# Optimization experiments

Measured on AMD Instinct MI355X. Metric: run time of the kernel, lower is better.

## Reference

```python
import jax, jax.numpy as jnp
import numpy as np
from jax import lax

NPOINT = 1024
RADIUS = 0.2
NSAMPLE = 32
BN_EPS = 1e-5


def farthest_point_sample(xyz, npoint):
    # xyz: (B, N, 3). Deterministic start at index 0 (torch version starts at a
    # random index; the algorithm is otherwise identical).
    B, N, _ = xyz.shape

    def step(carry, _):
        distance, farthest = carry
        centroid = jnp.take_along_axis(xyz, farthest[:, None, None], axis=1)  # (B,1,3)
        d = jnp.sum((xyz - centroid) ** 2, axis=-1)  # (B,N)
        distance = jnp.minimum(distance, d)
        new_farthest = jnp.argmax(distance, axis=-1).astype(jnp.int32)
        return (distance, new_farthest), farthest

    init = (jnp.full((B, N), 1e10, xyz.dtype), jnp.zeros((B,), jnp.int32))
    _, centroids = lax.scan(step, init, None, length=npoint)  # (npoint, B)
    return centroids.T  # (B, npoint)


def batched_gather(points, idx):
    # points: (B, N, C); idx: (B, ...) -> (B, ..., C)
    return jax.vmap(lambda p, i: p[i])(points, idx)


def square_distance(src, dst):
    # src: (B,S,3), dst: (B,N,3) -> (B,S,N)
    d = -2.0 * jnp.einsum('bsc,bnc->bsn', src, dst)
    d += jnp.sum(src ** 2, -1)[:, :, None]
    d += jnp.sum(dst ** 2, -1)[:, None, :]
    return d


def query_ball_point(radius, nsample, xyz, new_xyz):
    B, N, _ = xyz.shape
    S = new_xyz.shape[1]
    sqrdists = square_distance(new_xyz, xyz)                 # (B,S,N)
    neg_d, idx = lax.top_k(-sqrdists, nsample)               # smallest nsample dists
    out_of_ball = (-neg_d) > radius ** 2                     # (B,S,nsample)
    first = idx[:, :, 0]
    # if even the nearest point is outside the ball, group the centroid itself
    first = jnp.where(out_of_ball[:, :, 0], jnp.arange(S, dtype=idx.dtype)[None, :], first)
    idx = jnp.where(out_of_ball, first[:, :, None], idx)
    return idx


def sa_forward(xyz_b3n, points_bdn, params):
    xyz = jnp.transpose(xyz_b3n, (0, 2, 1))      # (B,N,3)
    pts = jnp.transpose(points_bdn, (0, 2, 1))   # (B,N,D)
    fps_idx = farthest_point_sample(xyz, NPOINT)             # (B,S)
    new_xyz = batched_gather(xyz, fps_idx)                   # (B,S,3)
    idx = query_ball_point(RADIUS, NSAMPLE, xyz, new_xyz)    # (B,S,K)
    grouped_xyz = batched_gather(xyz, idx)                   # (B,S,K,3)
    grouped_xyz_norm = grouped_xyz - new_xyz[:, :, None, :]
    grouped_pts = batched_gather(pts, idx)                   # (B,S,K,D)
    x = jnp.concatenate([grouped_xyz_norm, grouped_pts], -1) # (B,S,K,3+D)

    for (w, b, gamma, beta) in params:
        x = jnp.einsum('bskc,oc->bsko', x, w) + b            # 1x1 conv
        mu = jnp.mean(x, axis=(0, 1, 2))
        var = jnp.var(x, axis=(0, 1, 2))                     # biased, as torch BN
        x = jax.nn.relu(gamma * (x - mu) * lax.rsqrt(var + BN_EPS) + beta)

    new_points = jnp.max(x, axis=2)                          # max over nsample K
    return (jnp.transpose(new_xyz, (0, 2, 1)),
            jnp.transpose(new_points, (0, 2, 1)),
            fps_idx)


def setup_inputs() -> dict:
    key = jax.random.key(0)
    ks = jax.random.split(key, 8)
    B, N, D = 16, 4096, 64
    xyz = jax.random.uniform(ks[0], (B, 3, N), dtype=jnp.float32)
    points = jax.random.normal(ks[1], (B, D, N), dtype=jnp.float32)
    mlp = [64, 64, 128]
    last = 3 + D  # in_channel = 67
    inp = {'xyz': xyz, 'points': points}
    for i, out in enumerate(mlp):
        inp[f'w{i}'] = jax.random.normal(ks[2 + i], (out, last), dtype=jnp.float32) * (1.0 / np.sqrt(last))
        inp[f'b{i}'] = jnp.zeros((out,), jnp.float32)
        inp[f'gamma{i}'] = jnp.ones((out,), jnp.float32)
        inp[f'beta{i}'] = jnp.zeros((out,), jnp.float32)
        last = out
    return inp


def reference(xyz, points, w0, b0, gamma0, beta0, w1, b1, gamma1, beta1, w2, b2, gamma2, beta2):
    params = [(w0, b0, gamma0, beta0), (w1, b1, gamma1, beta1), (w2, b2, gamma2, beta2)]
    return sa_forward(xyz, points, params)
```

## Files before the change

### kernel.cpp

```cpp
#include <hip/hip_runtime.h>

using f32x4  = __attribute__((ext_vector_type(4))) float;
using short8 = __attribute__((ext_vector_type(8))) short;
using u64x2  = __attribute__((ext_vector_type(2))) unsigned long long;

__device__ __forceinline__ unsigned short f2bf(float f) {
  unsigned u = __builtin_bit_cast(unsigned, f);
  u = (u + 0x7FFFu + ((u >> 16) & 1u)) >> 16;
  return (unsigned short)u;
}
__device__ __forceinline__ float bf2f(unsigned short s) {
  return __builtin_bit_cast(float, ((unsigned)s) << 16);
}
__device__ __forceinline__ double u2d(unsigned long long u) {
  return __builtin_bit_cast(double, u);
}
__device__ __forceinline__ unsigned long long d2u(double d) {
  return __builtin_bit_cast(unsigned long long, d);
}
__device__ __forceinline__ unsigned cvt_pk_bf16(float lo, float hi) {
  unsigned r;
  asm("v_cvt_pk_bf16_f32 %0, %1, %2" : "=v"(r) : "v"(lo), "v"(hi));
  return r;
}

template <int CTRL>
__device__ __forceinline__ double dpp_max_f64(double best) {
  unsigned long long u = d2u(best);
  int lo32 = (int)(unsigned)u;
  int hi32 = (int)(unsigned)(u >> 32);
  int plo = __builtin_amdgcn_update_dpp(0, lo32, CTRL, 0xF, 0xF, true);
  int phi = __builtin_amdgcn_update_dpp(0, hi32, CTRL, 0xF, 0xF, true);
  unsigned long long p =
      ((unsigned long long)(unsigned)phi << 32) | (unsigned long long)(unsigned)plo;
  return fmax(best, u2d(p));
}
template <int CTRL>
__device__ __forceinline__ double dpp_min_f64(double v) {
  unsigned long long u = d2u(v);
  int lo32 = (int)(unsigned)u;
  int hi32 = (int)(unsigned)(u >> 32);
  int plo = __builtin_amdgcn_update_dpp(lo32, lo32, CTRL, 0xF, 0xF, false);
  int phi = __builtin_amdgcn_update_dpp(hi32, hi32, CTRL, 0xF, 0xF, false);
  unsigned long long p =
      ((unsigned long long)(unsigned)phi << 32) | (unsigned long long)(unsigned)plo;
  return fmin(v, u2d(p));
}

union SmemFP {
  struct {
    float4 sp4[4096];
    unsigned long long scand[2][16];
    int sfar[1024];
  } f;
  float tile[64][65];
};

__global__ __launch_bounds__(256, 1) void k_fp(const float* __restrict__ xyz,
                                               const float* __restrict__ points,
                                               float* __restrict__ out0,
                                               float* __restrict__ out2,
                                               int* __restrict__ fpsidx,
                                               float4* __restrict__ nq4,
                                               unsigned short* __restrict__ pT,
                                               float4* __restrict__ xyz4,
                                               const float* __restrict__ w0,
                                               const float* __restrict__ w1,
                                               const float* __restrict__ w2,
                                               unsigned short* __restrict__ wb0,
                                               unsigned short* __restrict__ wb1,
                                               unsigned short* __restrict__ wb2) {
  __shared__ SmemFP sm;
  int t = threadIdx.x, blk = blockIdx.x;
  if (blk >= 16) {
    int pb = blk - 16;
    if (pb == 1024) {
      for (int e = t; e < 64 * 96; e += 256) {
        int o = e / 96, k = e - o * 96;
        float v = (k < 64) ? w0[o * 67 + 3 + k] : ((k < 67) ? w0[o * 67 + (k - 64)] : 0.f);
        wb0[e] = f2bf(v);
      }
      for (int e = t; e < 4096; e += 256) wb1[e] = f2bf(w1[e]);
      for (int e = t; e < 8192; e += 256) wb2[e] = f2bf(w2[e]);
      return;
    }
    int b = pb >> 6, n0 = (pb & 63) << 6;
#pragma unroll
    for (int p = 0; p < 16; ++p) {
      int c = p * 4 + (t >> 6);
      sm.tile[c][t & 63] = points[(size_t)b * 262144 + (size_t)c * 4096 + n0 + (t & 63)];
    }
    if (t < 64) {
      int n = n0 + t;
      float x = xyz[(size_t)b * 12288 + n];
      float y = xyz[(size_t)b * 12288 + 4096 + n];
      float z = xyz[(size_t)b * 12288 + 8192 + n];
      float ps = __fadd_rn(__fadd_rn(__fmul_rn(x, x), __fmul_rn(y, y)), __fmul_rn(z, z));
      xyz4[(size_t)b * 4096 + n] = make_float4(x, y, z, ps);
    }
    __syncthreads();
    int nl = t >> 2, coff = (t & 3) * 16;
    unsigned v[8];
#pragma unroll
    for (int j = 0; j < 8; ++j)
      v[j] = cvt_pk_bf16(sm.tile[coff + 2 * j][nl], sm.tile[coff + 2 * j + 1][nl]);
    uint4* dst = reinterpret_cast<uint4*>(pT + ((size_t)b * 4096 + n0 + nl) * 64 + coff);
    dst[0] = make_uint4(v[0], v[1], v[2], v[3]);
    dst[1] = make_uint4(v[4], v[5], v[6], v[7]);
    return;
  }
  int b = blk;
  float px[16], py[16], pz[16], dist[16];
#pragma unroll
  for (int j = 0; j < 16; ++j) {
    int n = t + (j << 8);
    float x = xyz[(size_t)b * 12288 + n];
    float y = xyz[(size_t)b * 12288 + 4096 + n];
    float z = xyz[(size_t)b * 12288 + 8192 + n];
    px[j] = x; py[j] = y; pz[j] = z; dist[j] = 1e10f;
    sm.f.sp4[n] = make_float4(x, y, z, 0.f);
  }
  __syncthreads();
#pragma unroll
  for (int j = 0; j < 16; ++j) {
    asm volatile("" : "+v"(px[j]), "+v"(py[j]), "+v"(pz[j]));
  }
  unsigned nt = ~(unsigned)t;
  int far = 0;
  float cx = sm.f.sp4[0].x, cy = sm.f.sp4[0].y, cz = sm.f.sp4[0].z;
  for (int it = 0; it < 1024; ++it) {
    if (t == 0) sm.f.sfar[it] = far;
    double best0 = 0.0, best1 = 0.0;
#pragma unroll
    for (int j = 0; j < 16; ++j) {
      float dx = __fsub_rn(px[j], cx);
      float dy = __fsub_rn(py[j], cy);
      float dz = __fsub_rn(pz[j], cz);
      float d  = __fadd_rn(__fadd_rn(__fmul_rn(dx, dx), __fmul_rn(dy, dy)), __fmul_rn(dz, dz));
      float nd = fminf(dist[j], d);
      dist[j] = nd;
      unsigned long long cand =
          ((unsigned long long)__builtin_bit_cast(unsigned, nd) << 32) |
          (unsigned long long)(nt - (unsigned)(j << 8));
      if (j & 1) best1 = fmax(best1, u2d(cand));
      else       best0 = fmax(best0, u2d(cand));
    }
    double best = fmax(best0, best1);
    best = dpp_max_f64<0xB1>(best);
    best = dpp_max_f64<0x4E>(best);
    best = dpp_max_f64<0x124>(best);
    best = dpp_max_f64<0x128>(best);
    int pb = it & 1;
    if ((t & 15) == 0) sm.f.scand[pb][t >> 4] = d2u(best);
    __syncthreads();
    double g = u2d(sm.f.scand[pb][t & 15]);
    g = dpp_max_f64<0xB1>(g);
    g = dpp_max_f64<0x4E>(g);
    g = dpp_max_f64<0x124>(g);
    g = dpp_max_f64<0x128>(g);
    unsigned long long bw = d2u(g);
    int n = (int)(~(unsigned)bw) & 4095;
    far = n;
    float4 c4 = sm.f.sp4[n];
    cx = c4.x; cy = c4.y; cz = c4.z;
  }
  __syncthreads();
#pragma unroll
  for (int h = 0; h < 4; ++h) {
    int k = (h << 8) + t;
    int fr = sm.f.sfar[k];
    float4 p = sm.f.sp4[fr];
    float x = p.x, y = p.y, z = p.z;
    fpsidx[(b << 10) + k] = fr;
    out2[(b << 10) + k] = (float)fr;
    out0[(size_t)b * 3072 + k]        = x;
    out0[(size_t)b * 3072 + 1024 + k] = y;
    out0[(size_t)b * 3072 + 2048 + k] = z;
    float ps = __fadd_rn(__fadd_rn(__fmul_rn(x, x), __fmul_rn(y, y)), __fmul_rn(z, z));
    nq4[(b << 10) + k] = make_float4(x, y, z, ps);
  }
}

#define BCAP 384
__global__ __launch_bounds__(256) void k_ball(const float4* __restrict__ xyz4,
                                              const int* __restrict__ fpsidx,
                                              int* __restrict__ ballidx) {
  __shared__ __align__(16) float4 sp[4096];
  __shared__ unsigned long long spk[4][BCAP];
  const unsigned long long INVP = 0x7149F2CAFFFFFFFFull;
  int t = threadIdx.x, blk = blockIdx.x;
  int b = blk >> 6;
  for (int i = t; i < 4096; i += 256) sp[i] = xyz4[(size_t)b * 4096 + i];
  __syncthreads();
  int lane = t & 63, wid = t >> 6;
  for (int r = 0; r < 4; ++r) {
    int q = blk * 16 + r * 4 + wid;
    int qi = fpsidx[q];
    float4 Q = sp[qi];
    float qx = Q.x, qy = Q.y, qz = Q.z, qs = Q.w;
    int cnt = 0;
    for (int i = 0; i < 64; ++i) {
      int n = (i << 6) + lane;
      float4 P = sp[n];
      float dot = __fadd_rn(__fadd_rn(__fmul_rn(qx, P.x), __fmul_rn(qy, P.y)), __fmul_rn(qz, P.z));
      float d   = __fadd_rn(__fadd_rn(__fmul_rn(-2.f, dot), qs), P.w);
      bool in = (d <= 0.04f);
      unsigned long long m = __ballot(in);
      int pos = cnt + (int)__popcll(m & ((1ull << lane) - 1ull));
      if (in && pos < BCAP)
        spk[wid][pos] = ((unsigned long long)__builtin_bit_cast(unsigned, d) << 32) | (unsigned)n;
      cnt += (int)__popcll(m);
    }
    if (cnt > BCAP) cnt = BCAP;
    double c0, c1, c2, c3, c4, c5;
    {
      int s0 = lane, s1 = lane + 64, s2 = lane + 128, s3 = lane + 192, s4 = lane + 256, s5 = lane + 320;
      c0 = (s0 < cnt) ? u2d(spk[wid][s0]) : u2d(INVP);
      c1 = (s1 < cnt) ? u2d(spk[wid][s1]) : u2d(INVP);
      c2 = (s2 < cnt) ? u2d(spk[wid][s2]) : u2d(INVP);
      c3 = (s3 < cnt) ? u2d(spk[wid][s3]) : u2d(INVP);
      c4 = (s4 < cnt) ? u2d(spk[wid][s4]) : u2d(INVP);
      c5 = (s5 < cnt) ? u2d(spk[wid][s5]) : u2d(INVP);
    }
#define CE(a, b) { double mn_ = fmin(a, b), mx_ = fmax(a, b); a = mn_; b = mx_; }
    CE(c0, c1);
    CE(c1, c2); CE(c0, c1);
    CE(c2, c3); CE(c1, c2); CE(c0, c1);
    CE(c3, c4); CE(c2, c3); CE(c1, c2); CE(c0, c1);
    CE(c4, c5); CE(c3, c4); CE(c2, c3); CE(c1, c2); CE(c0, c1);
#undef CE
    int firstI = 0;
#pragma unroll 1
    for (int rr = 0; rr < 32; ++rr) {
      double h = c0;
      h = dpp_min_f64<0xB1>(h);
      h = dpp_min_f64<0x4E>(h);
      h = dpp_min_f64<0x124>(h);
      h = dpp_min_f64<0x128>(h);
      unsigned long long hu = d2u(h);
      int lo = (int)(unsigned)hu, hi = (int)(unsigned)(hu >> 32);
      unsigned long long r0 = ((unsigned long long)(unsigned)__builtin_amdgcn_readlane(hi, 0)  << 32) | (unsigned)__builtin_amdgcn_readlane(lo, 0);
      unsigned long long r1 = ((unsigned long long)(unsigned)__builtin_amdgcn_readlane(hi, 16) << 32) | (unsigned)__builtin_amdgcn_readlane(lo, 16);
      unsigned long long r2 = ((unsigned long long)(unsigned)__builtin_amdgcn_readlane(hi, 32) << 32) | (unsigned)__builtin_amdgcn_readlane(lo, 32);
      unsigned long long r3 = ((unsigned long long)(unsigned)__builtin_amdgcn_readlane(hi, 48) << 32) | (unsigned)__builtin_amdgcn_readlane(lo, 48);
      double w = fmin(fmin(u2d(r0), u2d(r1)), fmin(u2d(r2), u2d(r3)));
      unsigned long long wu = d2u(w);
      int wi = (int)(unsigned)wu;
      if (rr == 0) firstI = wi;
      int outv = (wu < INVP) ? wi : firstI;
      if (lane == 0) ballidx[(size_t)q * 32 + rr] = outv;
      if (d2u(c0) == wu) {
        c0 = c1; c1 = c2; c2 = c3; c3 = c4; c4 = c5; c5 = u2d(INVP);
      }
    }
  }
}

__global__ __launch_bounds__(256) void k_gemm1(const unsigned short* __restrict__ pT,
    const float4* __restrict__ xyz4, const float4* __restrict__ nq4,
    const int* __restrict__ bidx, const unsigned short* __restrict__ wb,
    const float* __restrict__ bia, unsigned short* __restrict__ xbuf,
    float* __restrict__ part) {
  __shared__ unsigned short A[64][104];
  __shared__ unsigned short W[64][104];
  __shared__ float sred[4][2][64];
  int t = threadIdx.x, blk = blockIdx.x;
  int b = blk >> 9;
  for (int e = t; e < 768; e += 256) {
    int o = e / 12, k8 = e - o * 12;
    *reinterpret_cast<uint4*>(&W[o][k8 * 8]) = reinterpret_cast<const uint4*>(wb)[e];
  }
  {
    int rt = t >> 2, sub = t & 3;
    int q = (blk << 1) + (rt >> 5);
    int n = bidx[(size_t)q * 32 + (rt & 31)];
    const uint4* src = reinterpret_cast<const uint4*>(pT + ((size_t)(b * 4096 + n)) * 64 + sub * 16);
    uint4 v0 = src[0], v1 = src[1];
    *reinterpret_cast<uint4*>(&A[rt][sub * 16])     = v0;
    *reinterpret_cast<uint4*>(&A[rt][sub * 16 + 8]) = v1;
    if (sub == 0) {
      float4 P = xyz4[(size_t)b * 4096 + n];
      float4 Qc = nq4[q];
      A[rt][64] = f2bf(__fsub_rn(P.x, Qc.x));
      A[rt][65] = f2bf(__fsub_rn(P.y, Qc.y));
      A[rt][66] = f2bf(__fsub_rn(P.z, Qc.z));
    } else if (sub == 1) {
#pragma unroll
      for (int k = 67; k < 96; ++k) A[rt][k] = 0;
    }
  }
  __syncthreads();
  int lane = t & 63, wid = t >> 6;
  int cl = lane & 15, rg = lane >> 4;
  int rowb = (wid << 4) + cl, ko = rg << 3;
  f32x4 acc[4] = {};
#pragma unroll
  for (int ks = 0; ks < 96; ks += 32) {
    short8 a = *reinterpret_cast<const short8*>(&A[rowb][ks + ko]);
#pragma unroll
    for (int nt = 0; nt < 4; ++nt) {
      short8 bb = *reinterpret_cast<const short8*>(&W[nt * 16 + cl][ks + ko]);
      acc[nt] = __builtin_amdgcn_mfma_f32_16x16x32_bf16(a, bb, acc[nt], 0, 0, 0);
    }
  }
#pragma unroll
  for (int nt = 0; nt < 4; ++nt) {
    int ch = nt * 16 + cl;
    float bv = bia[ch];
    float v0 = acc[nt][0] + bv, v1 = acc[nt][1] + bv, v2 = acc[nt][2] + bv, v3 = acc[nt][3] + bv;
    size_t gr = (size_t)blk * 64 + (wid << 4) + (rg << 2);
    xbuf[(gr + 0) * 64 + ch] = f2bf(v0);
    xbuf[(gr + 1) * 64 + ch] = f2bf(v1);
    xbuf[(gr + 2) * 64 + ch] = f2bf(v2);
    xbuf[(gr + 3) * 64 + ch] = f2bf(v3);
    float s1 = (v0 + v1) + (v2 + v3);
    float s2 = (v0 * v0 + v1 * v1) + (v2 * v2 + v3 * v3);
    s1 += __shfl_xor(s1, 16); s1 += __shfl_xor(s1, 32);
    s2 += __shfl_xor(s2, 16); s2 += __shfl_xor(s2, 32);
    if (rg == 0) { sred[wid][0][ch] = s1; sred[wid][1][ch] = s2; }
  }
  __syncthreads();
  if (t < 128) {
    int ch = t & 63, wh = t >> 6;
    float v = sred[0][wh][ch] + sred[1][wh][ch] + sred[2][wh][ch] + sred[3][wh][ch];
    part[(size_t)blk * 128 + ch * 2 + wh] = v;
  }
}

__global__ __launch_bounds__(256) void k_red(const float* __restrict__ part, int nblk, int nch,
    const float* __restrict__ gamma, const float* __restrict__ beta,
    float* __restrict__ scale, float* __restrict__ shift) {
  int c = blockIdx.x, t = threadIdx.x;
  int stride = 2 * nch;
  float s1 = 0.f, s2 = 0.f;
  for (int i = t; i < nblk; i += 256) {
    s1 += part[(size_t)i * stride + 2 * c];
    s2 += part[(size_t)i * stride + 2 * c + 1];
  }
  __shared__ float r1[256], r2[256];
  r1[t] = s1; r2[t] = s2;
  __syncthreads();
  for (int o = 128; o > 0; o >>= 1) {
    if (t < o) { r1[t] += r1[t + o]; r2[t] += r2[t + o]; }
    __syncthreads();
  }
  if (t == 0) {
    const float N = 524288.f;
    float mu = r1[0] / N;
    float var = r2[0] / N - mu * mu;
    float a = gamma[c] / sqrtf(var + 1e-5f);
    scale[c] = a;
    shift[c] = beta[c] - a * mu;
  }
}

__global__ __launch_bounds__(256) void k_gemm2(unsigned short* __restrict__ xbuf,
    const unsigned short* __restrict__ wb, const float* __restrict__ bia,
    const float* __restrict__ sc, const float* __restrict__ sh,
    float* __restrict__ part) {
  __shared__ unsigned short A[64][72];
  __shared__ unsigned short W[64][72];
  __shared__ float ssc[64], ssh[64];
  __shared__ float sred[4][2][64];
  int t = threadIdx.x, blk = blockIdx.x;
  if (t < 64) { ssc[t] = sc[t]; ssh[t] = sh[t]; }
  __syncthreads();
  for (int e = t; e < 512; e += 256) {
    int o = e >> 3, k8 = e & 7;
    *reinterpret_cast<uint4*>(&W[o][k8 * 8]) = reinterpret_cast<const uint4*>(wb)[e];
  }
  {
    int rt = t >> 2, sub = t & 3;
    size_t gr = (size_t)blk * 64 + rt;
    const uint4* src = reinterpret_cast<const uint4*>(xbuf + gr * 64 + sub * 16);
    uint4 v0 = src[0], v1 = src[1];
    unsigned wv[8] = {v0.x, v0.y, v0.z, v0.w, v1.x, v1.y, v1.z, v1.w};
    unsigned pk[8];
#pragma unroll
    for (int j = 0; j < 8; ++j) {
      int c = sub * 16 + 2 * j;
      float x0 = bf2f((unsigned short)(wv[j] & 0xffffu));
      float x1 = bf2f((unsigned short)(wv[j] >> 16));
      float a0 = fmaxf(0.f, ssc[c] * x0 + ssh[c]);
      float a1 = fmaxf(0.f, ssc[c + 1] * x1 + ssh[c + 1]);
      pk[j] = cvt_pk_bf16(a0, a1);
    }
    *reinterpret_cast<uint4*>(&A[rt][sub * 16])     = make_uint4(pk[0], pk[1], pk[2], pk[3]);
    *reinterpret_cast<uint4*>(&A[rt][sub * 16 + 8]) = make_uint4(pk[4], pk[5], pk[6], pk[7]);
  }
  __syncthreads();
  int lane = t & 63, wid = t >> 6;
  int cl = lane & 15, rg = lane >> 4;
  int rowb = (wid << 4) + cl, ko = rg << 3;
  f32x4 acc[4] = {};
#pragma unroll
  for (int ks = 0; ks < 64; ks += 32) {
    short8 a = *reinterpret_cast<const short8*>(&A[rowb][ks + ko]);
#pragma unroll
    for (int nt = 0; nt < 4; ++nt) {
      short8 bb = *reinterpret_cast<const short8*>(&W[nt * 16 + cl][ks + ko]);
      acc[nt] = __builtin_amdgcn_mfma_f32_16x16x32_bf16(a, bb, acc[nt], 0, 0, 0);
    }
  }
#pragma unroll
  for (int nt = 0; nt < 4; ++nt) {
    int ch = nt * 16 + cl;
    float bv = bia[ch];
    float v0 = acc[nt][0] + bv, v1 = acc[nt][1] + bv, v2 = acc[nt][2] + bv, v3 = acc[nt][3] + bv;
    size_t gr = (size_t)blk * 64 + (wid << 4) + (rg << 2);
    xbuf[(gr + 0) * 64 + ch] = f2bf(v0);
    xbuf[(gr + 1) * 64 + ch] = f2bf(v1);
    xbuf[(gr + 2) * 64 + ch] = f2bf(v2);
    xbuf[(gr + 3) * 64 + ch] = f2bf(v3);
    float s1 = (v0 + v1) + (v2 + v3);
    float s2 = (v0 * v0 + v1 * v1) + (v2 * v2 + v3 * v3);
    s1 += __shfl_xor(s1, 16); s1 += __shfl_xor(s1, 32);
    s2 += __shfl_xor(s2, 16); s2 += __shfl_xor(s2, 32);
    if (rg == 0) { sred[wid][0][ch] = s1; sred[wid][1][ch] = s2; }
  }
  __syncthreads();
  if (t < 128) {
    int ch = t & 63, wh = t >> 6;
    float v = sred[0][wh][ch] + sred[1][wh][ch] + sred[2][wh][ch] + sred[3][wh][ch];
    part[(size_t)blk * 128 + ch * 2 + wh] = v;
  }
}

__global__ __launch_bounds__(256) void k_gemm3(unsigned short* xbuf,
    const unsigned short* __restrict__ wb, const float* __restrict__ bia,
    const float* __restrict__ sc2, const float* __restrict__ sh2,
    float* __restrict__ part) {
  __shared__ unsigned short A[64][72];
  __shared__ unsigned short W[128][72];
  __shared__ float ssc[64], ssh[64];
  __shared__ float sred[4][4][128];
  int t = threadIdx.x, blk = blockIdx.x;
  if (t < 64) { ssc[t] = sc2[t]; ssh[t] = sh2[t]; }
  __syncthreads();
  for (int e = t; e < 1024; e += 256) {
    int o = e >> 3, k8 = e & 7;
    *reinterpret_cast<uint4*>(&W[o][k8 * 8]) = reinterpret_cast<const uint4*>(wb)[e];
  }
  {
    int rt = t >> 2, sub = t & 3;
    size_t gr = (size_t)blk * 64 + rt;
    const uint4* src = reinterpret_cast<const uint4*>(xbuf + gr * 64 + sub * 16);
    uint4 v0 = src[0], v1 = src[1];
    unsigned wv[8] = {v0.x, v0.y, v0.z, v0.w, v1.x, v1.y, v1.z, v1.w};
    unsigned pk[8];
#pragma unroll
    for (int j = 0; j < 8; ++j) {
      int c = sub * 16 + 2 * j;
      float x0 = bf2f((unsigned short)(wv[j] & 0xffffu));
      float x1 = bf2f((unsigned short)(wv[j] >> 16));
      float a0 = fmaxf(0.f, ssc[c] * x0 + ssh[c]);
      float a1 = fmaxf(0.f, ssc[c + 1] * x1 + ssh[c + 1]);
      pk[j] = cvt_pk_bf16(a0, a1);
    }
    *reinterpret_cast<uint4*>(&A[rt][sub * 16])     = make_uint4(pk[0], pk[1], pk[2], pk[3]);
    *reinterpret_cast<uint4*>(&A[rt][sub * 16 + 8]) = make_uint4(pk[4], pk[5], pk[6], pk[7]);
  }
  __syncthreads();
  int lane = t & 63, wid = t >> 6;
  int cl = lane & 15, rg = lane >> 4;
  int rowb = (wid << 4) + cl, ko = rg << 3;
  f32x4 acc[8] = {};
#pragma unroll
  for (int ks = 0; ks < 64; ks += 32) {
    short8 a = *reinterpret_cast<const short8*>(&A[rowb][ks + ko]);
#pragma unroll
    for (int nt = 0; nt < 8; ++nt) {
      short8 bb = *reinterpret_cast<const short8*>(&W[nt * 16 + cl][ks + ko]);
      acc[nt] = __builtin_amdgcn_mfma_f32_16x16x32_bf16(a, bb, acc[nt], 0, 0, 0);
    }
  }
#pragma unroll
  for (int nt = 0; nt < 8; ++nt) {
    int ch = nt * 16 + cl;
    float bv = bia[ch];
    float v0 = acc[nt][0] + bv, v1 = acc[nt][1] + bv, v2 = acc[nt][2] + bv, v3 = acc[nt][3] + bv;
    float s1 = (v0 + v1) + (v2 + v3);
    float s2 = (v0 * v0 + v1 * v1) + (v2 * v2 + v3 * v3);
    float mx = fmaxf(fmaxf(v0, v1), fmaxf(v2, v3));
    float mn = fminf(fminf(v0, v1), fminf(v2, v3));
    s1 += __shfl_xor(s1, 16); s1 += __shfl_xor(s1, 32);
    s2 += __shfl_xor(s2, 16); s2 += __shfl_xor(s2, 32);
    mx = fmaxf(mx, __shfl_xor(mx, 16)); mx = fmaxf(mx, __shfl_xor(mx, 32));
    mn = fminf(mn, __shfl_xor(mn, 16)); mn = fminf(mn, __shfl_xor(mn, 32));
    if (rg == 0) {
      sred[wid][0][ch] = s1; sred[wid][1][ch] = s2;
      sred[wid][2][ch] = mx; sred[wid][3][ch] = mn;
    }
  }
  __syncthreads();
  {
    int ch = t & 127, wh = t >> 7;
    part[(size_t)blk * 256 + ch * 2 + wh] =
        sred[0][wh][ch] + sred[1][wh][ch] + sred[2][wh][ch] + sred[3][wh][ch];
    float mx = fmaxf(sred[2 * wh][2][ch], sred[2 * wh + 1][2][ch]);
    float mn = fminf(sred[2 * wh][3][ch], sred[2 * wh + 1][3][ch]);
    float* mm = reinterpret_cast<float*>(xbuf) + (size_t)blk * 2048;
    mm[wh * 256 + ch]       = mx;
    mm[wh * 256 + 128 + ch] = mn;
  }
}

__global__ __launch_bounds__(256) void k_fin(const float* __restrict__ mm,
                                             const float* __restrict__ sc3,
                                             const float* __restrict__ sh3,
                                             float* __restrict__ out1) {
  __shared__ float tile[32][33];
  int t = threadIdx.x, blk = blockIdx.x;
  int b = blk >> 7, rem = blk & 127, ct = rem >> 5, st = rem & 31;
  int c0 = ct * 32, s0 = st * 32;
#pragma unroll
  for (int p = 0; p < 4; ++p) {
    int s_local = (t >> 5) + p * 8;
    int c = c0 + (t & 31);
    int q = (b << 10) + s0 + s_local;
    size_t base = (size_t)(q >> 1) * 2048 + (size_t)(q & 1) * 256;
    float mx = mm[base + c];
    float mn = mm[base + 128 + c];
    float sc = sc3[c], sh = sh3[c];
    float v = (sc >= 0.f) ? mx : mn;
    tile[t & 31][s_local] = fmaxf(0.f, sc * v + sh);
  }
  __syncthreads();
#pragma unroll
  for (int p = 0; p < 4; ++p) {
    int c = c0 + (t >> 5) + p * 8;
    int s = s0 + (t & 31);
    out1[(size_t)b * 131072 + (size_t)c * 1024 + s] = tile[(t >> 5) + p * 8][t & 31];
  }
}

extern "C" void kernel_launch(void* const* d_in, const int* in_sizes, int n_in,
                              void* d_out, int out_size, void* d_ws, size_t ws_size,
                              hipStream_t stream) {
  (void)in_sizes; (void)n_in; (void)out_size;
  const float* xyz    = (const float*)d_in[0];
  const float* points = (const float*)d_in[1];
  const float* w0  = (const float*)d_in[2];
  const float* b0  = (const float*)d_in[3];
  const float* g0  = (const float*)d_in[4];
  const float* be0 = (const float*)d_in[5];
  const float* w1  = (const float*)d_in[6];
  const float* b1  = (const float*)d_in[7];
  const float* g1  = (const float*)d_in[8];
  const float* be1 = (const float*)d_in[9];
  const float* w2  = (const float*)d_in[10];
  const float* b2  = (const float*)d_in[11];
  const float* g2  = (const float*)d_in[12];
  const float* be2 = (const float*)d_in[13];
  float* out  = (float*)d_out;
  float* out0 = out;
  float* out1 = out + 49152;
  float* out2 = out + 49152 + 2097152;
  char* ws = (char*)d_ws;
  const size_t OFF_PT    = 0;
  const size_t OFF_XYZ4  = 8388608;
  const size_t OFF_NQ4   = 9437184;
  const size_t OFF_FPS   = 9699328;
  const size_t OFF_BALL  = 9764864;
  const size_t OFF_XBUF  = 11862016;
  const size_t OFF_PART  = 78970880;
  const size_t OFF_SC    = 87359488;
  const size_t OFF_WB    = 87363584;
  const size_t NEED      = 87400448;
  if (ws_size < NEED) return;
  unsigned short* pT   = (unsigned short*)(ws + OFF_PT);
  float4* xyz4 = (float4*)(ws + OFF_XYZ4);
  float4* nq4  = (float4*)(ws + OFF_NQ4);
  int* fpsidx  = (int*)(ws + OFF_FPS);
  int* ballidx = (int*)(ws + OFF_BALL);
  unsigned short* xbuf = (unsigned short*)(ws + OFF_XBUF);
  float* part  = (float*)(ws + OFF_PART);
  float* scb   = (float*)(ws + OFF_SC);
  float *sc1 = scb, *sh1 = scb + 128, *sc2 = scb + 256, *sh2 = scb + 384,
        *sc3 = scb + 512, *sh3 = scb + 640;
  unsigned short* wb0 = (unsigned short*)(ws + OFF_WB);
  unsigned short* wb1 = wb0 + 6144;
  unsigned short* wb2 = wb1 + 4096;

  k_fp<<<1041, 256, 0, stream>>>(xyz, points, out0, out2, fpsidx, nq4,
                                 pT, xyz4, w0, w1, w2, wb0, wb1, wb2);
  k_ball<<<1024, 256, 0, stream>>>(xyz4, fpsidx, ballidx);
  k_gemm1<<<8192, 256, 0, stream>>>(pT, xyz4, nq4, ballidx, wb0, b0, xbuf, part);
  k_red<<<64, 256, 0, stream>>>(part, 8192, 64, g0, be0, sc1, sh1);
  k_gemm2<<<8192, 256, 0, stream>>>(xbuf, wb1, b1, sc1, sh1, part);
  k_red<<<64, 256, 0, stream>>>(part, 8192, 64, g1, be1, sc2, sh2);
  k_gemm3<<<8192, 256, 0, stream>>>(xbuf, wb2, b2, sc2, sh2, part);
  k_red<<<128, 256, 0, stream>>>(part, 8192, 128, g2, be2, sc3, sh3);
  k_fin<<<2048, 256, 0, stream>>>((const float*)xbuf, sc3, sh3, out1);
}
```

Baseline: 814.8 us.

## Recompute earlier MLP layers per stage instead of storing intermediate activations

Replaces the store-and-reload of bf16 intermediate activations between the three MLP stages with recomputation. Each stage re-gathers the grouped inputs and recomputes the previous GEMMs in shared memory before its own GEMM and batch-norm statistics. This removes about 64 MB of activation writes and reads per layer pass. In exchange it adds redundant MFMA work, repeated gathers and more shared memory per block, which may reduce occupancy.

```diff
diff --git a/kernel.cpp b/kernel.cpp
--- a/kernel.cpp
+++ b/kernel.cpp
@@ -256,11 +256,34 @@
   }
 }
 
-__global__ __launch_bounds__(256) void k_gemm1(const unsigned short* __restrict__ pT,
+template <typename SmemA>
+__device__ __forceinline__ void build_A(SmemA& A, int blk, int b,
+    const unsigned short* __restrict__ pT, const float4* __restrict__ xyz4,
+    const float4* __restrict__ nq4, const int* __restrict__ bidx) {
+  int t = threadIdx.x;
+  int rt = t >> 2, sub = t & 3;
+  int q = (blk << 1) + (rt >> 5);
+  int n = bidx[(size_t)q * 32 + (rt & 31)];
+  const uint4* src = reinterpret_cast<const uint4*>(pT + ((size_t)(b * 4096 + n)) * 64 + sub * 16);
+  uint4 v0 = src[0], v1 = src[1];
+  *reinterpret_cast<uint4*>(&A[rt][sub * 16])     = v0;
+  *reinterpret_cast<uint4*>(&A[rt][sub * 16 + 8]) = v1;
+  if (sub == 0) {
+    float4 P = xyz4[(size_t)b * 4096 + n];
+    float4 Qc = nq4[q];
+    A[rt][64] = f2bf(__fsub_rn(P.x, Qc.x));
+    A[rt][65] = f2bf(__fsub_rn(P.y, Qc.y));
+    A[rt][66] = f2bf(__fsub_rn(P.z, Qc.z));
+  } else if (sub == 1) {
+#pragma unroll
+    for (int k = 67; k < 96; ++k) A[rt][k] = 0;
+  }
+}
+
+__global__ __launch_bounds__(256) void k_g1s(const unsigned short* __restrict__ pT,
     const float4* __restrict__ xyz4, const float4* __restrict__ nq4,
     const int* __restrict__ bidx, const unsigned short* __restrict__ wb,
-    const float* __restrict__ bia, unsigned short* __restrict__ xbuf,
-    float* __restrict__ part) {
+    const float* __restrict__ bia, float* __restrict__ part) {
   __shared__ unsigned short A[64][104];
   __shared__ unsigned short W[64][104];
   __shared__ float sred[4][2][64];
@@ -270,25 +293,7 @@
     int o = e / 12, k8 = e - o * 12;
     *reinterpret_cast<uint4*>(&W[o][k8 * 8]) = reinterpret_cast<const uint4*>(wb)[e];
   }
-  {
-    int rt = t >> 2, sub = t & 3;
-    int q = (blk << 1) + (rt >> 5);
-    int n = bidx[(size_t)q * 32 + (rt & 31)];
-    const uint4* src = reinterpret_cast<const uint4*>(pT + ((size_t)(b * 4096 + n)) * 64 + sub * 16);
-    uint4 v0 = src[0], v1 = src[1];
-    *reinterpret_cast<uint4*>(&A[rt][sub * 16])     = v0;
-    *reinterpret_cast<uint4*>(&A[rt][sub * 16 + 8]) = v1;
-    if (sub == 0) {
-      float4 P = xyz4[(size_t)b * 4096 + n];
-      float4 Qc = nq4[q];
-      A[rt][64] = f2bf(__fsub_rn(P.x, Qc.x));
-      A[rt][65] = f2bf(__fsub_rn(P.y, Qc.y));
-      A[rt][66] = f2bf(__fsub_rn(P.z, Qc.z));
-    } else if (sub == 1) {
-#pragma unroll
-      for (int k = 67; k < 96; ++k) A[rt][k] = 0;
-    }
-  }
+  build_A(A, blk, b, pT, xyz4, nq4, bidx);
   __syncthreads();
   int lane = t & 63, wid = t >> 6;
   int cl = lane & 15, rg = lane >> 4;
@@ -308,11 +313,6 @@
     int ch = nt * 16 + cl;
     float bv = bia[ch];
     float v0 = acc[nt][0] + bv, v1 = acc[nt][1] + bv, v2 = acc[nt][2] + bv, v3 = acc[nt][3] + bv;
-    size_t gr = (size_t)blk * 64 + (wid << 4) + (rg << 2);
-    xbuf[(gr + 0) * 64 + ch] = f2bf(v0);
-    xbuf[(gr + 1) * 64 + ch] = f2bf(v1);
-    xbuf[(gr + 2) * 64 + ch] = f2bf(v2);
-    xbuf[(gr + 3) * 64 + ch] = f2bf(v3);
     float s1 = (v0 + v1) + (v2 + v3);
     float s2 = (v0 * v0 + v1 * v1) + (v2 * v2 + v3 * v3);
     s1 += __shfl_xor(s1, 16); s1 += __shfl_xor(s1, 32);
@@ -327,91 +327,75 @@
   }
 }
 
-__global__ __launch_bounds__(256) void k_red(const float* __restrict__ part, int nblk, int nch,
-    const float* __restrict__ gamma, const float* __restrict__ beta,
-    float* __restrict__ scale, float* __restrict__ shift) {
-  int c = blockIdx.x, t = threadIdx.x;
-  int stride = 2 * nch;
-  float s1 = 0.f, s2 = 0.f;
-  for (int i = t; i < nblk; i += 256) {
-    s1 += part[(size_t)i * stride + 2 * c];
-    s2 += part[(size_t)i * stride + 2 * c + 1];
-  }
-  __shared__ float r1[256], r2[256];
-  r1[t] = s1; r2[t] = s2;
-  __syncthreads();
-  for (int o = 128; o > 0; o >>= 1) {
-    if (t < o) { r1[t] += r1[t + o]; r2[t] += r2[t + o]; }
-    __syncthreads();
-  }
-  if (t == 0) {
-    const float N = 524288.f;
-    float mu = r1[0] / N;
-    float var = r2[0] / N - mu * mu;
-    float a = gamma[c] / sqrtf(var + 1e-5f);
-    scale[c] = a;
-    shift[c] = beta[c] - a * mu;
-  }
-}
-
-__global__ __launch_bounds__(256) void k_gemm2(unsigned short* __restrict__ xbuf,
-    const unsigned short* __restrict__ wb, const float* __restrict__ bia,
-    const float* __restrict__ sc, const float* __restrict__ sh,
+__global__ __launch_bounds__(256) void k_g2r(const unsigned short* __restrict__ pT,
+    const float4* __restrict__ xyz4, const float4* __restrict__ nq4,
+    const int* __restrict__ bidx,
+    const unsigned short* __restrict__ wb0, const float* __restrict__ bia0,
+    const unsigned short* __restrict__ wb1, const float* __restrict__ bia1,
+    const float* __restrict__ sc1, const float* __restrict__ sh1,
     float* __restrict__ part) {
-  __shared__ unsigned short A[64][72];
-  __shared__ unsigned short W[64][72];
+  __shared__ unsigned short A[64][104];
+  __shared__ unsigned short W1[64][104];
+  __shared__ unsigned short W2[64][72];
   __shared__ float ssc[64], ssh[64];
   __shared__ float sred[4][2][64];
   int t = threadIdx.x, blk = blockIdx.x;
-  if (t < 64) { ssc[t] = sc[t]; ssh[t] = sh[t]; }
-  __syncthreads();
+  int b = blk >> 9;
+  if (t < 64) { ssc[t] = sc1[t]; ssh[t] = sh1[t]; }
+  for (int e = t; e < 768; e += 256) {
+    int o = e / 12, k8 = e - o * 12;
+    *reinterpret_cast<uint4*>(&W1[o][k8 * 8]) = reinterpret_cast<const uint4*>(wb0)[e];
+  }
   for (int e = t; e < 512; e += 256) {
     int o = e >> 3, k8 = e & 7;
-    *reinterpret_cast<uint4*>(&W[o][k8 * 8]) = reinterpret_cast<const uint4*>(wb)[e];
-  }
-  {
-    int rt = t >> 2, sub = t & 3;
-    size_t gr = (size_t)blk * 64 + rt;
-    const uint4* src = reinterpret_cast<const uint4*>(xbuf + gr * 64 + sub * 16);
-    uint4 v0 = src[0], v1 = src[1];
-    unsigned wv[8] = {v0.x, v0.y, v0.z, v0.w, v1.x, v1.y, v1.z, v1.w};
-    unsigned pk[8];
-#pragma unroll
-    for (int j = 0; j < 8; ++j) {
-      int c = sub * 16 + 2 * j;
-      float x0 = bf2f((unsigned short)(wv[j] & 0xffffu));
-      float x1 = bf2f((unsigned short)(wv[j] >> 16));
-      float a0 = fmaxf(0.f, ssc[c] * x0 + ssh[c]);
-      float a1 = fmaxf(0.f, ssc[c + 1] * x1 + ssh[c + 1]);
-      pk[j] = cvt_pk_bf16(a0, a1);
-    }
-    *reinterpret_cast<uint4*>(&A[rt][sub * 16])     = make_uint4(pk[0], pk[1], pk[2], pk[3]);
-    *reinterpret_cast<uint4*>(&A[rt][sub * 16 + 8]) = make_uint4(pk[4], pk[5], pk[6], pk[7]);
-  }
+    *reinterpret_cast<uint4*>(&W2[o][k8 * 8]) = reinterpret_cast<const uint4*>(wb1)[e];
+  }
+  build_A(A, blk, b, pT, xyz4, nq4, bidx);
   __syncthreads();
   int lane = t & 63, wid = t >> 6;
   int cl = lane & 15, rg = lane >> 4;
   int rowb = (wid << 4) + cl, ko = rg << 3;
-  f32x4 acc[4] = {};
+  f32x4 acc1[4] = {};
+#pragma unroll
+  for (int ks = 0; ks < 96; ks += 32) {
+    short8 a = *reinterpret_cast<const short8*>(&A[rowb][ks + ko]);
+#pragma unroll
+    for (int nt = 0; nt < 4; ++nt) {
+      short8 bb = *reinterpret_cast<const short8*>(&W1[nt * 16 + cl][ks + ko]);
+      acc1[nt] = __builtin_amdgcn_mfma_f32_16x16x32_bf16(a, bb, acc1[nt], 0, 0, 0);
+    }
+  }
+  __syncthreads();
+  {
+    int r0 = (wid << 4) + (rg << 2);
+#pragma unroll
+    for (int nt = 0; nt < 4; ++nt) {
+      int ch = nt * 16 + cl;
+      float bv = bia0[ch];
+#pragma unroll
+      for (int i = 0; i < 4; ++i) {
+        float x1 = bf2f(f2bf(acc1[nt][i] + bv));
+        float a = fmaxf(0.f, ssc[ch] * x1 + ssh[ch]);
+        A[r0 + i][ch] = f2bf(a);
+      }
+    }
+  }
+  __syncthreads();
+  f32x4 acc2[4] = {};
 #pragma unroll
   for (int ks = 0; ks < 64; ks += 32) {
     short8 a = *reinterpret_cast<const short8*>(&A[rowb][ks + ko]);
 #pragma unroll
     for (int nt = 0; nt < 4; ++nt) {
-      short8 bb = *reinterpret_cast<const short8*>(&W[nt * 16 + cl][ks + ko]);
-      acc[nt] = __builtin_amdgcn_mfma_f32_16x16x32_bf16(a, bb, acc[nt], 0, 0, 0);
+      short8 bb = *reinterpret_cast<const short8*>(&W2[nt * 16 + cl][ks + ko]);
+      acc2[nt] = __builtin_amdgcn_mfma_f32_16x16x32_bf16(a, bb, acc2[nt], 0, 0, 0);
     }
   }
 #pragma unroll
   for (int nt = 0; nt < 4; ++nt) {
     int ch = nt * 16 + cl;
-    float bv = bia[ch];
-    float v0 = acc[nt][0] + bv, v1 = acc[nt][1] + bv, v2 = acc[nt][2] + bv, v3 = acc[nt][3] + bv;
-    size_t gr = (size_t)blk * 64 + (wid << 4) + (rg << 2);
-    xbuf[(gr + 0) * 64 + ch] = f2bf(v0);
-    xbuf[(gr + 1) * 64 + ch] = f2bf(v1);
-    xbuf[(gr + 2) * 64 + ch] = f2bf(v2);
-    xbuf[(gr + 3) * 64 + ch] = f2bf(v3);
+    float bv = bia1[ch];
+    float v0 = acc2[nt][0] + bv, v1 = acc2[nt][1] + bv, v2 = acc2[nt][2] + bv, v3 = acc2[nt][3] + bv;
     float s1 = (v0 + v1) + (v2 + v3);
     float s2 = (v0 * v0 + v1 * v1) + (v2 * v2 + v3 * v3);
     s1 += __shfl_xor(s1, 16); s1 += __shfl_xor(s1, 32);
@@ -426,59 +410,104 @@
   }
 }
 
-__global__ __launch_bounds__(256) void k_gemm3(unsigned short* xbuf,
-    const unsigned short* __restrict__ wb, const float* __restrict__ bia,
+__global__ __launch_bounds__(256) void k_g3r(const unsigned short* __restrict__ pT,
+    const float4* __restrict__ xyz4, const float4* __restrict__ nq4,
+    const int* __restrict__ bidx,
+    const unsigned short* __restrict__ wb0, const float* __restrict__ bia0,
+    const unsigned short* __restrict__ wb1, const float* __restrict__ bia1,
+    const unsigned short* __restrict__ wb2, const float* __restrict__ bia2,
+    const float* __restrict__ sc1, const float* __restrict__ sh1,
     const float* __restrict__ sc2, const float* __restrict__ sh2,
-    float* __restrict__ part) {
-  __shared__ unsigned short A[64][72];
-  __shared__ unsigned short W[128][72];
-  __shared__ float ssc[64], ssh[64];
+    float* __restrict__ mmout, float* __restrict__ part) {
+  __shared__ unsigned short A[64][104];
+  __shared__ unsigned short W1[64][104];
+  __shared__ unsigned short W2[64][72];
+  __shared__ unsigned short W3[128][72];
+  __shared__ float s1c[64], s1h[64], s2c[64], s2h[64];
   __shared__ float sred[4][4][128];
   int t = threadIdx.x, blk = blockIdx.x;
-  if (t < 64) { ssc[t] = sc2[t]; ssh[t] = sh2[t]; }
-  __syncthreads();
+  int b = blk >> 9;
+  if (t < 64) { s1c[t] = sc1[t]; s1h[t] = sh1[t]; }
+  else if (t < 128) { s2c[t - 64] = sc2[t - 64]; s2h[t - 64] = sh2[t - 64]; }
+  for (int e = t; e < 768; e += 256) {
+    int o = e / 12, k8 = e - o * 12;
+    *reinterpret_cast<uint4*>(&W1[o][k8 * 8]) = reinterpret_cast<const uint4*>(wb0)[e];
+  }
+  for (int e = t; e < 512; e += 256) {
+    int o = e >> 3, k8 = e & 7;
+    *reinterpret_cast<uint4*>(&W2[o][k8 * 8]) = reinterpret_cast<const uint4*>(wb1)[e];
+  }
   for (int e = t; e < 1024; e += 256) {
     int o = e >> 3, k8 = e & 7;
-    *reinterpret_cast<uint4*>(&W[o][k8 * 8]) = reinterpret_cast<const uint4*>(wb)[e];
-  }
-  {
-    int rt = t >> 2, sub = t & 3;
-    size_t gr = (size_t)blk * 64 + rt;
-    const uint4* src = reinterpret_cast<const uint4*>(xbuf + gr * 64 + sub * 16);
-    uint4 v0 = src[0], v1 = src[1];
-    unsigned wv[8] = {v0.x, v0.y, v0.z, v0.w, v1.x, v1.y, v1.z, v1.w};
-    unsigned pk[8];
-#pragma unroll
-    for (int j = 0; j < 8; ++j) {
-      int c = sub * 16 + 2 * j;
-      float x0 = bf2f((unsigned short)(wv[j] & 0xffffu));
-      float x1 = bf2f((unsigned short)(wv[j] >> 16));
-      float a0 = fmaxf(0.f, ssc[c] * x0 + ssh[c]);
-      float a1 = fmaxf(0.f, ssc[c + 1] * x1 + ssh[c + 1]);
-      pk[j] = cvt_pk_bf16(a0, a1);
-    }
-    *reinterpret_cast<uint4*>(&A[rt][sub * 16])     = make_uint4(pk[0], pk[1], pk[2], pk[3]);
-    *reinterpret_cast<uint4*>(&A[rt][sub * 16 + 8]) = make_uint4(pk[4], pk[5], pk[6], pk[7]);
-  }
+    *reinterpret_cast<uint4*>(&W3[o][k8 * 8]) = reinterpret_cast<const uint4*>(wb2)[e];
+  }
+  build_A(A, blk, b, pT, xyz4, nq4, bidx);
   __syncthreads();
   int lane = t & 63, wid = t >> 6;
   int cl = lane & 15, rg = lane >> 4;
   int rowb = (wid << 4) + cl, ko = rg << 3;
-  f32x4 acc[8] = {};
+  int r0 = (wid << 4) + (rg << 2);
+  f32x4 acc1[4] = {};
+#pragma unroll
+  for (int ks = 0; ks < 96; ks += 32) {
+    short8 a = *reinterpret_cast<const short8*>(&A[rowb][ks + ko]);
+#pragma unroll
+    for (int nt = 0; nt < 4; ++nt) {
+      short8 bb = *reinterpret_cast<const short8*>(&W1[nt * 16 + cl][ks + ko]);
+      acc1[nt] = __builtin_amdgcn_mfma_f32_16x16x32_bf16(a, bb, acc1[nt], 0, 0, 0);
+    }
+  }
+  __syncthreads();
+#pragma unroll
+  for (int nt = 0; nt < 4; ++nt) {
+    int ch = nt * 16 + cl;
+    float bv = bia0[ch];
+#pragma unroll
+    for (int i = 0; i < 4; ++i) {
+      float x1 = bf2f(f2bf(acc1[nt][i] + bv));
+      float a = fmaxf(0.f, s1c[ch] * x1 + s1h[ch]);
+      A[r0 + i][ch] = f2bf(a);
+    }
+  }
+  __syncthreads();
+  f32x4 acc2[4] = {};
 #pragma unroll
   for (int ks = 0; ks < 64; ks += 32) {
     short8 a = *reinterpret_cast<const short8*>(&A[rowb][ks + ko]);
 #pragma unroll
+    for (int nt = 0; nt < 4; ++nt) {
+      short8 bb = *reinterpret_cast<const short8*>(&W2[nt * 16 + cl][ks + ko]);
+      acc2[nt] = __builtin_amdgcn_mfma_f32_16x16x32_bf16(a, bb, acc2[nt], 0, 0, 0);
+    }
+  }
+  __syncthreads();
+#pragma unroll
+  for (int nt = 0; nt < 4; ++nt) {
+    int ch = nt * 16 + cl;
+    float bv = bia1[ch];
+#pragma unroll
+    for (int i = 0; i < 4; ++i) {
+      float x2 = bf2f(f2bf(acc2[nt][i] + bv));
+      float a = fmaxf(0.f, s2c[ch] * x2 + s2h[ch]);
+      A[r0 + i][ch] = f2bf(a);
+    }
+  }
+  __syncthreads();
+  f32x4 acc3[8] = {};
+#pragma unroll
+  for (int ks = 0; ks < 64; ks += 32) {
+    short8 a = *reinterpret_cast<const short8*>(&A[rowb][ks + ko]);
+#pragma unroll
     for (int nt = 0; nt < 8; ++nt) {
-      short8 bb = *reinterpret_cast<const short8*>(&W[nt * 16 + cl][ks + ko]);
-      acc[nt] = __builtin_amdgcn_mfma_f32_16x16x32_bf16(a, bb, acc[nt], 0, 0, 0);
+      short8 bb = *reinterpret_cast<const short8*>(&W3[nt * 16 + cl][ks + ko]);
+      acc3[nt] = __builtin_amdgcn_mfma_f32_16x16x32_bf16(a, bb, acc3[nt], 0, 0, 0);
     }
   }
 #pragma unroll
   for (int nt = 0; nt < 8; ++nt) {
     int ch = nt * 16 + cl;
-    float bv = bia[ch];
-    float v0 = acc[nt][0] + bv, v1 = acc[nt][1] + bv, v2 = acc[nt][2] + bv, v3 = acc[nt][3] + bv;
+    float bv = bia2[ch];
+    float v0 = acc3[nt][0] + bv, v1 = acc3[nt][1] + bv, v2 = acc3[nt][2] + bv, v3 = acc3[nt][3] + bv;
     float s1 = (v0 + v1) + (v2 + v3);
     float s2 = (v0 * v0 + v1 * v1) + (v2 * v2 + v3 * v3);
     float mx = fmaxf(fmaxf(v0, v1), fmaxf(v2, v3));
@@ -499,9 +528,36 @@
         sred[0][wh][ch] + sred[1][wh][ch] + sred[2][wh][ch] + sred[3][wh][ch];
     float mx = fmaxf(sred[2 * wh][2][ch], sred[2 * wh + 1][2][ch]);
     float mn = fminf(sred[2 * wh][3][ch], sred[2 * wh + 1][3][ch]);
-    float* mm = reinterpret_cast<float*>(xbuf) + (size_t)blk * 2048;
+    float* mm = mmout + (size_t)blk * 2048;
     mm[wh * 256 + ch]       = mx;
     mm[wh * 256 + 128 + ch] = mn;
+  }
+}
+
+__global__ __launch_bounds__(256) void k_red(const float* __restrict__ part, int nblk, int nch,
+    const float* __restrict__ gamma, const float* __restrict__ beta,
+    float* __restrict__ scale, float* __restrict__ shift) {
+  int c = blockIdx.x, t = threadIdx.x;
+  int stride = 2 * nch;
+  float s1 = 0.f, s2 = 0.f;
+  for (int i = t; i < nblk; i += 256) {
+    s1 += part[(size_t)i * stride + 2 * c];
+    s2 += part[(size_t)i * stride + 2 * c + 1];
+  }
+  __shared__ float r1[256], r2[256];
+  r1[t] = s1; r2[t] = s2;
+  __syncthreads();
+  for (int o = 128; o > 0; o >>= 1) {
+    if (t < o) { r1[t] += r1[t + o]; r2[t] += r2[t + o]; }
+    __syncthreads();
+  }
+  if (t == 0) {
+    const float N = 524288.f;
+    float mu = r1[0] / N;
+    float var = r2[0] / N - mu * mu;
+    float a = gamma[c] / sqrtf(var + 1e-5f);
+    scale[c] = a;
+    shift[c] = beta[c] - a * mu;
   }
 }
 
@@ -562,7 +618,7 @@
   const size_t OFF_NQ4   = 9437184;
   const size_t OFF_FPS   = 9699328;
   const size_t OFF_BALL  = 9764864;
-  const size_t OFF_XBUF  = 11862016;
+  const size_t OFF_MM    = 11862016;
   const size_t OFF_PART  = 78970880;
   const size_t OFF_SC    = 87359488;
   const size_t OFF_WB    = 87363584;
@@ -573,7 +629,7 @@
   float4* nq4  = (float4*)(ws + OFF_NQ4);
   int* fpsidx  = (int*)(ws + OFF_FPS);
   int* ballidx = (int*)(ws + OFF_BALL);
-  unsigned short* xbuf = (unsigned short*)(ws + OFF_XBUF);
+  float* mmbuf = (float*)(ws + OFF_MM);
   float* part  = (float*)(ws + OFF_PART);
   float* scb   = (float*)(ws + OFF_SC);
   float *sc1 = scb, *sh1 = scb + 128, *sc2 = scb + 256, *sh2 = scb + 384,
@@ -585,11 +641,12 @@
   k_fp<<<1041, 256, 0, stream>>>(xyz, points, out0, out2, fpsidx, nq4,
                                  pT, xyz4, w0, w1, w2, wb0, wb1, wb2);
   k_ball<<<1024, 256, 0, stream>>>(xyz4, fpsidx, ballidx);
-  k_gemm1<<<8192, 256, 0, stream>>>(pT, xyz4, nq4, ballidx, wb0, b0, xbuf, part);
+  k_g1s<<<8192, 256, 0, stream>>>(pT, xyz4, nq4, ballidx, wb0, b0, part);
   k_red<<<64, 256, 0, stream>>>(part, 8192, 64, g0, be0, sc1, sh1);
-  k_gemm2<<<8192, 256, 0, stream>>>(xbuf, wb1, b1, sc1, sh1, part);
+  k_g2r<<<8192, 256, 0, stream>>>(pT, xyz4, nq4, ballidx, wb0, b0, wb1, b1, sc1, sh1, part);
   k_red<<<64, 256, 0, stream>>>(part, 8192, 64, g1, be1, sc2, sh2);
-  k_gemm3<<<8192, 256, 0, stream>>>(xbuf, wb2, b2, sc2, sh2, part);
+  k_g3r<<<8192, 256, 0, stream>>>(pT, xyz4, nq4, ballidx, wb0, b0, wb1, b1, wb2, b2,
+                                  sc1, sh1, sc2, sh2, mmbuf, part);
   k_red<<<128, 256, 0, stream>>>(part, 8192, 128, g2, be2, sc3, sh3);
-  k_fin<<<2048, 256, 0, stream>>>((const float*)xbuf, sc3, sh3, out1);
-}
+  k_fin<<<2048, 256, 0, stream>>>(mmbuf, sc3, sh3, out1);
+}
```

Result: slower. 897.8 us (+10.2%).

## Recompute layer-2 GEMM inside layer-3 kernel instead of storing activations

Applied to the files above, without the earlier changes.

The layer-2 kernel now only computes BN statistics and no longer writes its bf16 output back to the activation buffer. The layer-3 kernel reloads the layer-1 output, recomputes layer 2 (GEMM, bias, bf16 rounding, BN, ReLU) in shared memory, and then runs layer 3. This removes one full write of the 64-channel activation buffer and its reread, at the cost of doing the layer-2 GEMM twice and using more shared memory per block, which may lower occupancy.

```diff
diff --git a/kernel.cpp b/kernel.cpp
--- a/kernel.cpp
+++ b/kernel.cpp
@@ -354,7 +354,7 @@
   }
 }
 
-__global__ __launch_bounds__(256) void k_gemm2(unsigned short* __restrict__ xbuf,
+__global__ __launch_bounds__(256) void k_g2s(const unsigned short* __restrict__ xbuf,
     const unsigned short* __restrict__ wb, const float* __restrict__ bia,
     const float* __restrict__ sc, const float* __restrict__ sh,
     float* __restrict__ part) {
@@ -407,11 +407,6 @@
     int ch = nt * 16 + cl;
     float bv = bia[ch];
     float v0 = acc[nt][0] + bv, v1 = acc[nt][1] + bv, v2 = acc[nt][2] + bv, v3 = acc[nt][3] + bv;
-    size_t gr = (size_t)blk * 64 + (wid << 4) + (rg << 2);
-    xbuf[(gr + 0) * 64 + ch] = f2bf(v0);
-    xbuf[(gr + 1) * 64 + ch] = f2bf(v1);
-    xbuf[(gr + 2) * 64 + ch] = f2bf(v2);
-    xbuf[(gr + 3) * 64 + ch] = f2bf(v3);
     float s1 = (v0 + v1) + (v2 + v3);
     float s2 = (v0 * v0 + v1 * v1) + (v2 * v2 + v3 * v3);
     s1 += __shfl_xor(s1, 16); s1 += __shfl_xor(s1, 32);
@@ -426,20 +421,28 @@
   }
 }
 
-__global__ __launch_bounds__(256) void k_gemm3(unsigned short* xbuf,
-    const unsigned short* __restrict__ wb, const float* __restrict__ bia,
+__global__ __launch_bounds__(256) void k_g3x(unsigned short* xbuf,
+    const unsigned short* __restrict__ wb1, const float* __restrict__ bia1,
+    const unsigned short* __restrict__ wb2, const float* __restrict__ bia2,
+    const float* __restrict__ sc1, const float* __restrict__ sh1,
     const float* __restrict__ sc2, const float* __restrict__ sh2,
     float* __restrict__ part) {
   __shared__ unsigned short A[64][72];
-  __shared__ unsigned short W[128][72];
-  __shared__ float ssc[64], ssh[64];
+  __shared__ unsigned short W2[64][72];
+  __shared__ unsigned short W3[128][72];
+  __shared__ float s1c[64], s1h[64], s2c[64], s2h[64];
   __shared__ float sred[4][4][128];
   int t = threadIdx.x, blk = blockIdx.x;
-  if (t < 64) { ssc[t] = sc2[t]; ssh[t] = sh2[t]; }
-  __syncthreads();
+  if (t < 64) { s1c[t] = sc1[t]; s1h[t] = sh1[t]; }
+  else if (t < 128) { s2c[t - 64] = sc2[t - 64]; s2h[t - 64] = sh2[t - 64]; }
+  __syncthreads();
+  for (int e = t; e < 512; e += 256) {
+    int o = e >> 3, k8 = e & 7;
+    *reinterpret_cast<uint4*>(&W2[o][k8 * 8]) = reinterpret_cast<const uint4*>(wb1)[e];
+  }
   for (int e = t; e < 1024; e += 256) {
     int o = e >> 3, k8 = e & 7;
-    *reinterpret_cast<uint4*>(&W[o][k8 * 8]) = reinterpret_cast<const uint4*>(wb)[e];
+    *reinterpret_cast<uint4*>(&W3[o][k8 * 8]) = reinterpret_cast<const uint4*>(wb2)[e];
   }
   {
     int rt = t >> 2, sub = t & 3;
@@ -453,8 +456,8 @@
       int c = sub * 16 + 2 * j;
       float x0 = bf2f((unsigned short)(wv[j] & 0xffffu));
       float x1 = bf2f((unsigned short)(wv[j] >> 16));
-      float a0 = fmaxf(0.f, ssc[c] * x0 + ssh[c]);
-      float a1 = fmaxf(0.f, ssc[c + 1] * x1 + ssh[c + 1]);
+      float a0 = fmaxf(0.f, s1c[c] * x0 + s1h[c]);
+      float a1 = fmaxf(0.f, s1c[c + 1] * x1 + s1h[c + 1]);
       pk[j] = cvt_pk_bf16(a0, a1);
     }
     *reinterpret_cast<uint4*>(&A[rt][sub * 16])     = make_uint4(pk[0], pk[1], pk[2], pk[3]);
@@ -464,21 +467,45 @@
   int lane = t & 63, wid = t >> 6;
   int cl = lane & 15, rg = lane >> 4;
   int rowb = (wid << 4) + cl, ko = rg << 3;
-  f32x4 acc[8] = {};
+  int r0 = (wid << 4) + (rg << 2);
+  f32x4 acc2[4] = {};
 #pragma unroll
   for (int ks = 0; ks < 64; ks += 32) {
     short8 a = *reinterpret_cast<const short8*>(&A[rowb][ks + ko]);
 #pragma unroll
+    for (int nt = 0; nt < 4; ++nt) {
+      short8 bb = *reinterpret_cast<const short8*>(&W2[nt * 16 + cl][ks + ko]);
+      acc2[nt] = __builtin_amdgcn_mfma_f32_16x16x32_bf16(a, bb, acc2[nt], 0, 0, 0);
+    }
+  }
+  __syncthreads();
+#pragma unroll
+  for (int nt = 0; nt < 4; ++nt) {
+    int ch = nt * 16 + cl;
+    float bv = bia1[ch];
+#pragma unroll
+    for (int i = 0; i < 4; ++i) {
+      float x2 = bf2f(f2bf(acc2[nt][i] + bv));
+      float a = fmaxf(0.f, s2c[ch] * x2 + s2h[ch]);
+      A[r0 + i][ch] = f2bf(a);
+    }
+  }
+  __syncthreads();
+  f32x4 acc3[8] = {};
+#pragma unroll
+  for (int ks = 0; ks < 64; ks += 32) {
+    short8 a = *reinterpret_cast<const short8*>(&A[rowb][ks + ko]);
+#pragma unroll
     for (int nt = 0; nt < 8; ++nt) {
-      short8 bb = *reinterpret_cast<const short8*>(&W[nt * 16 + cl][ks + ko]);
-      acc[nt] = __builtin_amdgcn_mfma_f32_16x16x32_bf16(a, bb, acc[nt], 0, 0, 0);
+      short8 bb = *reinterpret_cast<const short8*>(&W3[nt * 16 + cl][ks + ko]);
+      acc3[nt] = __builtin_amdgcn_mfma_f32_16x16x32_bf16(a, bb, acc3[nt], 0, 0, 0);
     }
   }
 #pragma unroll
   for (int nt = 0; nt < 8; ++nt) {
     int ch = nt * 16 + cl;
-    float bv = bia[ch];
-    float v0 = acc[nt][0] + bv, v1 = acc[nt][1] + bv, v2 = acc[nt][2] + bv, v3 = acc[nt][3] + bv;
+    float bv = bia2[ch];
+    float v0 = acc3[nt][0] + bv, v1 = acc3[nt][1] + bv, v2 = acc3[nt][2] + bv, v3 = acc3[nt][3] + bv;
     float s1 = (v0 + v1) + (v2 + v3);
     float s2 = (v0 * v0 + v1 * v1) + (v2 * v2 + v3 * v3);
     float mx = fmaxf(fmaxf(v0, v1), fmaxf(v2, v3));
@@ -587,9 +614,9 @@
   k_ball<<<1024, 256, 0, stream>>>(xyz4, fpsidx, ballidx);
   k_gemm1<<<8192, 256, 0, stream>>>(pT, xyz4, nq4, ballidx, wb0, b0, xbuf, part);
   k_red<<<64, 256, 0, stream>>>(part, 8192, 64, g0, be0, sc1, sh1);
-  k_gemm2<<<8192, 256, 0, stream>>>(xbuf, wb1, b1, sc1, sh1, part);
+  k_g2s<<<8192, 256, 0, stream>>>(xbuf, wb1, b1, sc1, sh1, part);
   k_red<<<64, 256, 0, stream>>>(part, 8192, 64, g1, be1, sc2, sh2);
-  k_gemm3<<<8192, 256, 0, stream>>>(xbuf, wb2, b2, sc2, sh2, part);
+  k_g3x<<<8192, 256, 0, stream>>>(xbuf, wb1, b1, wb2, b2, sc1, sh1, sc2, sh2, part);
   k_red<<<128, 256, 0, stream>>>(part, 8192, 128, g2, be2, sc3, sh3);
   k_fin<<<2048, 256, 0, stream>>>((const float*)xbuf, sc3, sh3, out1);
 }
```

After: 830.2 us. No clear change (+1.9%).
